# Kernel optimization log

Measured on AMD Instinct MI355X. Metric: run time of the kernel, lower is better.

The kernel has to match this reference:

```python
import jax, jax.numpy as jnp
import numpy as np

B, W, H = 8, 1024, 1024
NUM_LABELS = 100  # mask ids in [0, NUM_LABELS); 0 = background
EPS = 1e-7


def setup_inputs() -> dict:
    key = jax.random.key(0)
    k1, k2 = jax.random.split(key)
    pred = jax.random.normal(k1, (B, 2, W, H), dtype=jnp.float32)
    mask = jax.random.randint(k2, (B, W, H), 0, NUM_LABELS, dtype=jnp.int32)
    ignored_map = jnp.ones((B, W, H), dtype=jnp.float32)
    return {"pred": pred, "mask": mask, "ignored_map": ignored_map}


def _smooth_l1(d):
    # SmoothL1Loss(reduction='none'), beta=1
    a = jnp.abs(d)
    return jnp.where(a < 1.0, 0.5 * d * d, a - 0.5)


def _gt_single(mask2d):
    # Vectorized replacement of the per-instance python loop:
    # segment-mean for centroids, segment-max for the per-instance `norm`.
    seg = mask2d.reshape(-1)  # [W*H]
    x_map = jnp.tile(jnp.arange(H, dtype=jnp.float32), W)    # column index (x)
    y_map = jnp.repeat(jnp.arange(W, dtype=jnp.float32), H)  # row index (y)
    cnt = jax.ops.segment_sum(jnp.ones_like(x_map), seg, num_segments=NUM_LABELS)
    safe_cnt = jnp.maximum(cnt, 1.0)
    xc = (jax.ops.segment_sum(x_map, seg, num_segments=NUM_LABELS) / safe_cnt)[seg]
    yc = (jax.ops.segment_sum(y_map, seg, num_segments=NUM_LABELS) / safe_cnt)[seg]
    fg = (seg != 0).astype(jnp.float32)  # label 0 is background (index_list[1:])
    vx = (x_map - xc) * fg  # (x_map - mean_x) * nuclei, instances are disjoint
    vy = (y_map - yc) * fg
    # torch.max over the whole image of (coord - c)*nuclei == max(seg_max, 0)
    mx = jnp.maximum(jax.ops.segment_max(vx, seg, num_segments=NUM_LABELS), 0.0)
    my = jnp.maximum(jax.ops.segment_max(vy, seg, num_segments=NUM_LABELS), 0.0)
    gx = vx / jnp.where(mx == 0.0, 1.0, mx)[seg]  # norm(): divide by max iff max != 0
    gy = vy / jnp.where(my == 0.0, 1.0, my)[seg]
    return jnp.stack([gx, gy]).reshape(2, W, H)


def reference(pred, mask, ignored_map):
    gt = jax.vmap(_gt_single)(mask)  # [B, 2, W, H]
    fg = (mask != 0).astype(jnp.float32)[:, None]  # [B, 1, W, H]
    bg = 1.0 - fg
    n = float(mask.size)
    # ((mask != 0) + 1e-07).sum() == fg_count + eps * numel
    fg_den = jnp.sum(fg) + EPS * n
    bg_den = jnp.sum(bg) + EPS * n
    d = _smooth_l1(pred - gt)
    ig = ignored_map[:, None]
    offset_loss = jnp.sum(d * ig * (fg / fg_den + bg / bg_den))
    return offset_loss, gt
```

## Files before the change

kernel.cpp:

```cpp
#include <hip/hip_runtime.h>

#define NL 100
#define BB 8
#define WW 1024
#define HH 1024
#define NPIX (WW * WW)
#define EPSF 1e-7f

#define OFF_CNT 0
#define OFF_SX  800
#define OFF_SY  1600
#define OFF_XC  2400
#define OFF_YC  3200
#define OFF_MX  4000
#define OFF_MY  4800
#define OFF_INV 5600
#define WS_WORDS 5602

__global__ __launch_bounds__(256) void k_hist(const int* __restrict__ mask,
                                              int* __restrict__ ws) {
    __shared__ int s_cnt[4][NL];
    __shared__ int s_sx[4][NL];
    __shared__ int s_sy[4][NL];
    const int b  = blockIdx.y;
    const int wv = threadIdx.x >> 6;
    for (int i = threadIdx.x; i < 4 * NL; i += 256) {
        ((int*)s_cnt)[i] = 0; ((int*)s_sx)[i] = 0; ((int*)s_sy)[i] = 0;
    }
    __syncthreads();
    const int4* m4 = (const int4*)(mask + (size_t)b * NPIX);
    const int base4 = blockIdx.x * 1024;
#pragma unroll
    for (int it = 0; it < 4; ++it) {
        const int i4 = base4 + it * 256 + threadIdx.x;
        const int4 mv = m4[i4];
        const int p  = i4 << 2;
        const int x0 = p & (HH - 1);
        const int y  = p >> 10;
        atomicAdd(&s_cnt[wv][mv.x], 1); atomicAdd(&s_sx[wv][mv.x], x0);     atomicAdd(&s_sy[wv][mv.x], y);
        atomicAdd(&s_cnt[wv][mv.y], 1); atomicAdd(&s_sx[wv][mv.y], x0 + 1); atomicAdd(&s_sy[wv][mv.y], y);
        atomicAdd(&s_cnt[wv][mv.z], 1); atomicAdd(&s_sx[wv][mv.z], x0 + 2); atomicAdd(&s_sy[wv][mv.z], y);
        atomicAdd(&s_cnt[wv][mv.w], 1); atomicAdd(&s_sx[wv][mv.w], x0 + 3); atomicAdd(&s_sy[wv][mv.w], y);
    }
    __syncthreads();
    for (int i = threadIdx.x; i < NL; i += 256) {
        const int c = s_cnt[0][i] + s_cnt[1][i] + s_cnt[2][i] + s_cnt[3][i];
        if (c) {
            atomicAdd(&ws[OFF_CNT + b * NL + i], c);
            atomicAdd(&ws[OFF_SX  + b * NL + i], s_sx[0][i] + s_sx[1][i] + s_sx[2][i] + s_sx[3][i]);
            atomicAdd(&ws[OFF_SY  + b * NL + i], s_sy[0][i] + s_sy[1][i] + s_sy[2][i] + s_sy[3][i]);
        }
    }
}

__global__ void k_final(int* __restrict__ wsi) {
    float* wsf = (float*)wsi;
    const int t = threadIdx.x;
    if (t < BB * NL) {
        const int c = wsi[OFF_CNT + t];
        const float sc = (float)(c > 0 ? c : 1);
        wsf[OFF_XC + t] = (float)wsi[OFF_SX + t] / sc;
        wsf[OFF_YC + t] = (float)wsi[OFF_SY + t] / sc;
    }
    if (t == 0) {
        long long bg = 0;
        for (int b = 0; b < BB; ++b) bg += wsi[OFF_CNT + b * NL];
        const float n = (float)BB * (float)NPIX;
        const float fg_den = (float)((long long)BB * NPIX - bg) + EPSF * n;
        const float bg_den = (float)bg + EPSF * n;
        wsf[OFF_INV + 0] = 1.0f / fg_den;
        wsf[OFF_INV + 1] = 1.0f / bg_den;
    }
}

__global__ __launch_bounds__(256) void k_max(const int* __restrict__ mask,
                                             int* __restrict__ ws) {
    const float* wsf = (const float*)ws;
    __shared__ float s_xc[NL], s_yc[NL];
    __shared__ unsigned s_mx[4][NL], s_my[4][NL];
    const int b  = blockIdx.y;
    const int wv = threadIdx.x >> 6;
    for (int i = threadIdx.x; i < NL; i += 256) {
        s_xc[i] = wsf[OFF_XC + b * NL + i];
        s_yc[i] = wsf[OFF_YC + b * NL + i];
    }
    for (int i = threadIdx.x; i < 4 * NL; i += 256) {
        ((unsigned*)s_mx)[i] = 0u; ((unsigned*)s_my)[i] = 0u;
    }
    __syncthreads();
    const int4* m4 = (const int4*)(mask + (size_t)b * NPIX);
    const int base4 = blockIdx.x * 1024;
#pragma unroll
    for (int it = 0; it < 4; ++it) {
        const int i4 = base4 + it * 256 + threadIdx.x;
        const int4 mv = m4[i4];
        const int p  = i4 << 2;
        const float x0 = (float)(p & (HH - 1));
        const float y  = (float)(p >> 10);
        const int mm[4] = {mv.x, mv.y, mv.z, mv.w};
#pragma unroll
        for (int j = 0; j < 4; ++j) {
            const int m = mm[j];
            if (m != 0) {
                const float vx = x0 + (float)j - s_xc[m];
                const float vy = y - s_yc[m];
                if (vx > 0.0f) atomicMax(&s_mx[wv][m], __float_as_uint(vx));
                if (vy > 0.0f) atomicMax(&s_my[wv][m], __float_as_uint(vy));
            }
        }
    }
    __syncthreads();
    for (int i = threadIdx.x; i < NL; i += 256) {
        const unsigned ax = max(max(s_mx[0][i], s_mx[1][i]), max(s_mx[2][i], s_mx[3][i]));
        const unsigned ay = max(max(s_my[0][i], s_my[1][i]), max(s_my[2][i], s_my[3][i]));
        if (ax) atomicMax((unsigned*)&ws[OFF_MX + b * NL + i], ax);
        if (ay) atomicMax((unsigned*)&ws[OFF_MY + b * NL + i], ay);
    }
}

__global__ __launch_bounds__(256) void k_loss(const int* __restrict__ mask,
                                              const float* __restrict__ pred,
                                              const float* __restrict__ ig,
                                              const int* __restrict__ ws,
                                              float* __restrict__ out) {
    const float* wsf = (const float*)ws;
    __shared__ float s_xc[NL], s_yc[NL], s_imx[NL], s_imy[NL];
    const int b = blockIdx.y;
    for (int i = threadIdx.x; i < NL; i += 256) {
        s_xc[i] = wsf[OFF_XC + b * NL + i];
        s_yc[i] = wsf[OFF_YC + b * NL + i];
        const float mx = wsf[OFF_MX + b * NL + i];
        const float my = wsf[OFF_MY + b * NL + i];
        s_imx[i] = (mx == 0.0f) ? 1.0f : 1.0f / mx;
        s_imy[i] = (my == 0.0f) ? 1.0f : 1.0f / my;
    }
    __syncthreads();
    const float inv_fg = wsf[OFF_INV + 0];
    const float inv_bg = wsf[OFF_INV + 1];
    const int4*   m4  = (const int4*)(mask + (size_t)b * NPIX);
    const float4* ig4 = (const float4*)(ig + (size_t)b * NPIX);
    const float4* px4 = (const float4*)(pred + (size_t)(b * 2) * NPIX);
    const float4* py4 = (const float4*)(pred + (size_t)(b * 2 + 1) * NPIX);
    float* gx_out = out + 1 + (size_t)(b * 2) * NPIX;
    float* gy_out = out + 1 + (size_t)(b * 2 + 1) * NPIX;

    float acc = 0.0f;
    const int base4 = blockIdx.x * 1024;
#pragma unroll
    for (int it = 0; it < 4; ++it) {
        const int i4 = base4 + it * 256 + threadIdx.x;
        const int4   mv  = m4[i4];
        const float4 iv  = ig4[i4];
        const float4 pxv = px4[i4];
        const float4 pyv = py4[i4];
        const int p  = i4 << 2;
        const float x0 = (float)(p & (HH - 1));
        const float y  = (float)(p >> 10);
        const int*   mm  = (const int*)&mv;
        const float* igs = (const float*)&iv;
        const float* pxs = (const float*)&pxv;
        const float* pys = (const float*)&pyv;
#pragma unroll
        for (int j = 0; j < 4; ++j) {
            const int m = mm[j];
            float gx = 0.0f, gy = 0.0f, w;
            if (m != 0) {
                gx = (x0 + (float)j - s_xc[m]) * s_imx[m];
                gy = (y - s_yc[m]) * s_imy[m];
                w = inv_fg;
            } else {
                w = inv_bg;
            }
            w *= igs[j];
            const float dx = pxs[j] - gx;
            const float dy = pys[j] - gy;
            const float ax = fabsf(dx), ay = fabsf(dy);
            const float lx = (ax < 1.0f) ? 0.5f * dx * dx : ax - 0.5f;
            const float ly = (ay < 1.0f) ? 0.5f * dy * dy : ay - 0.5f;
            acc += (lx + ly) * w;
            gx_out[p + j] = gx;
            gy_out[p + j] = gy;
        }
    }
#pragma unroll
    for (int off = 32; off > 0; off >>= 1) acc += __shfl_down(acc, off, 64);
    __shared__ float s_part[4];
    const int lane = threadIdx.x & 63, wv = threadIdx.x >> 6;
    if (lane == 0) s_part[wv] = acc;
    __syncthreads();
    if (threadIdx.x == 0) atomicAdd(out, s_part[0] + s_part[1] + s_part[2] + s_part[3]);
}

extern "C" void kernel_launch(void* const* d_in, const int* in_sizes, int n_in,
                              void* d_out, int out_size, void* d_ws, size_t ws_size,
                              hipStream_t stream) {
    const float* pred = (const float*)d_in[0];
    const int*   mask = (const int*)d_in[1];
    const float* ig   = (const float*)d_in[2];
    float* out = (float*)d_out;
    int*   ws  = (int*)d_ws;

    hipMemsetAsync(d_ws, 0, WS_WORDS * sizeof(int), stream);
    hipMemsetAsync(d_out, 0, sizeof(float), stream);

    dim3 grid(256, BB);
    k_hist<<<grid, 256, 0, stream>>>(mask, ws);
    k_final<<<1, 800, 0, stream>>>(ws);
    k_max<<<grid, 256, 0, stream>>>(mask, ws);
    k_loss<<<grid, 256, 0, stream>>>(mask, pred, ig, ws, out);
}
```

Measured before the change: 216.2 us.

## Fold max pass into stats via max(coord)-centroid identity, pack histogram atomics

```diff
diff --git a/kernel.cpp b/kernel.cpp
--- a/kernel.cpp
+++ b/kernel.cpp
@@ -4,52 +4,70 @@
 #define BB 8
 #define WW 1024
 #define HH 1024
-#define NPIX (WW * WW)
+#define NPIX (WW * HH)
 #define EPSF 1e-7f
 
 #define OFF_CNT 0
 #define OFF_SX  800
 #define OFF_SY  1600
-#define OFF_XC  2400
-#define OFF_YC  3200
-#define OFF_MX  4000
-#define OFF_MY  4800
-#define OFF_INV 5600
-#define WS_WORDS 5602
+#define OFF_MX  2400
+#define OFF_MY  3200
+#define OFF_TAB 4000
+#define OFF_INV 7200
+#define WS_WORDS 7202
 
-__global__ __launch_bounds__(256) void k_hist(const int* __restrict__ mask,
-                                              int* __restrict__ ws) {
-    __shared__ int s_cnt[4][NL];
-    __shared__ int s_sx[4][NL];
-    __shared__ int s_sy[4][NL];
+__global__ __launch_bounds__(256) void k_stats(const int* __restrict__ mask,
+                                               int* __restrict__ ws) {
+    __shared__ unsigned long long s_h[4][NL];
+    __shared__ int s_mx[4][NL];
+    __shared__ int s_my[4][NL];
     const int b  = blockIdx.y;
     const int wv = threadIdx.x >> 6;
     for (int i = threadIdx.x; i < 4 * NL; i += 256) {
-        ((int*)s_cnt)[i] = 0; ((int*)s_sx)[i] = 0; ((int*)s_sy)[i] = 0;
+        ((unsigned long long*)s_h)[i] = 0ull;
+        ((int*)s_mx)[i] = 0;
+        ((int*)s_my)[i] = 0;
     }
     __syncthreads();
     const int4* m4 = (const int4*)(mask + (size_t)b * NPIX);
-    const int base4 = blockIdx.x * 1024;
+    const int base4 = blockIdx.x * 2048;
 #pragma unroll
-    for (int it = 0; it < 4; ++it) {
+    for (int it = 0; it < 8; ++it) {
         const int i4 = base4 + it * 256 + threadIdx.x;
         const int4 mv = m4[i4];
         const int p  = i4 << 2;
         const int x0 = p & (HH - 1);
         const int y  = p >> 10;
-        atomicAdd(&s_cnt[wv][mv.x], 1); atomicAdd(&s_sx[wv][mv.x], x0);     atomicAdd(&s_sy[wv][mv.x], y);
-        atomicAdd(&s_cnt[wv][mv.y], 1); atomicAdd(&s_sx[wv][mv.y], x0 + 1); atomicAdd(&s_sy[wv][mv.y], y);
-        atomicAdd(&s_cnt[wv][mv.z], 1); atomicAdd(&s_sx[wv][mv.z], x0 + 2); atomicAdd(&s_sy[wv][mv.z], y);
-        atomicAdd(&s_cnt[wv][mv.w], 1); atomicAdd(&s_sx[wv][mv.w], x0 + 3); atomicAdd(&s_sy[wv][mv.w], y);
+        const int mm[4] = {mv.x, mv.y, mv.z, mv.w};
+#pragma unroll
+        for (int j = 0; j < 4; ++j) {
+            const int m = mm[j];
+            const int x = x0 + j;
+            atomicAdd(&s_h[wv][m],
+                      (1ull << 46) | ((unsigned long long)x << 23) | (unsigned long long)y);
+            if (x > s_mx[wv][m]) atomicMax(&s_mx[wv][m], x);
+            if (y > s_my[wv][m]) atomicMax(&s_my[wv][m], y);
+        }
     }
     __syncthreads();
     for (int i = threadIdx.x; i < NL; i += 256) {
-        const int c = s_cnt[0][i] + s_cnt[1][i] + s_cnt[2][i] + s_cnt[3][i];
+        int c = 0, sx = 0, sy = 0, mx = 0, my = 0;
+#pragma unroll
+        for (int w = 0; w < 4; ++w) {
+            const unsigned long long v = s_h[w][i];
+            c  += (int)(v >> 46);
+            sx += (int)((v >> 23) & 0x7FFFFFull);
+            sy += (int)(v & 0x7FFFFFull);
+            mx = max(mx, s_mx[w][i]);
+            my = max(my, s_my[w][i]);
+        }
         if (c) {
             atomicAdd(&ws[OFF_CNT + b * NL + i], c);
-            atomicAdd(&ws[OFF_SX  + b * NL + i], s_sx[0][i] + s_sx[1][i] + s_sx[2][i] + s_sx[3][i]);
-            atomicAdd(&ws[OFF_SY  + b * NL + i], s_sy[0][i] + s_sy[1][i] + s_sy[2][i] + s_sy[3][i]);
+            atomicAdd(&ws[OFF_SX  + b * NL + i], sx);
+            atomicAdd(&ws[OFF_SY  + b * NL + i], sy);
         }
+        if (mx) atomicMax(&ws[OFF_MX + b * NL + i], mx);
+        if (my) atomicMax(&ws[OFF_MY + b * NL + i], my);
     }
 }
 
@@ -59,8 +77,16 @@
     if (t < BB * NL) {
         const int c = wsi[OFF_CNT + t];
         const float sc = (float)(c > 0 ? c : 1);
-        wsf[OFF_XC + t] = (float)wsi[OFF_SX + t] / sc;
-        wsf[OFF_YC + t] = (float)wsi[OFF_SY + t] / sc;
+        const float xc = (float)wsi[OFF_SX + t] / sc;
+        const float yc = (float)wsi[OFF_SY + t] / sc;
+        float fmx = (float)wsi[OFF_MX + t] - xc; if (fmx < 0.0f) fmx = 0.0f;
+        float fmy = (float)wsi[OFF_MY + t] - yc; if (fmy < 0.0f) fmy = 0.0f;
+        float4 e;
+        e.x = xc;
+        e.y = yc;
+        e.z = (fmx == 0.0f) ? 1.0f : 1.0f / fmx;
+        e.w = (fmy == 0.0f) ? 1.0f : 1.0f / fmy;
+        ((float4*)(wsf + OFF_TAB))[t] = e;
     }
     if (t == 0) {
         long long bg = 0;
@@ -73,115 +99,62 @@
     }
 }
 
-__global__ __launch_bounds__(256) void k_max(const int* __restrict__ mask,
-                                             int* __restrict__ ws) {
-    const float* wsf = (const float*)ws;
-    __shared__ float s_xc[NL], s_yc[NL];
-    __shared__ unsigned s_mx[4][NL], s_my[4][NL];
-    const int b  = blockIdx.y;
-    const int wv = threadIdx.x >> 6;
-    for (int i = threadIdx.x; i < NL; i += 256) {
-        s_xc[i] = wsf[OFF_XC + b * NL + i];
-        s_yc[i] = wsf[OFF_YC + b * NL + i];
-    }
-    for (int i = threadIdx.x; i < 4 * NL; i += 256) {
-        ((unsigned*)s_mx)[i] = 0u; ((unsigned*)s_my)[i] = 0u;
-    }
-    __syncthreads();
-    const int4* m4 = (const int4*)(mask + (size_t)b * NPIX);
-    const int base4 = blockIdx.x * 1024;
-#pragma unroll
-    for (int it = 0; it < 4; ++it) {
-        const int i4 = base4 + it * 256 + threadIdx.x;
-        const int4 mv = m4[i4];
-        const int p  = i4 << 2;
-        const float x0 = (float)(p & (HH - 1));
-        const float y  = (float)(p >> 10);
-        const int mm[4] = {mv.x, mv.y, mv.z, mv.w};
-#pragma unroll
-        for (int j = 0; j < 4; ++j) {
-            const int m = mm[j];
-            if (m != 0) {
-                const float vx = x0 + (float)j - s_xc[m];
-                const float vy = y - s_yc[m];
-                if (vx > 0.0f) atomicMax(&s_mx[wv][m], __float_as_uint(vx));
-                if (vy > 0.0f) atomicMax(&s_my[wv][m], __float_as_uint(vy));
-            }
-        }
-    }
-    __syncthreads();
-    for (int i = threadIdx.x; i < NL; i += 256) {
-        const unsigned ax = max(max(s_mx[0][i], s_mx[1][i]), max(s_mx[2][i], s_mx[3][i]));
-        const unsigned ay = max(max(s_my[0][i], s_my[1][i]), max(s_my[2][i], s_my[3][i]));
-        if (ax) atomicMax((unsigned*)&ws[OFF_MX + b * NL + i], ax);
-        if (ay) atomicMax((unsigned*)&ws[OFF_MY + b * NL + i], ay);
-    }
-}
-
 __global__ __launch_bounds__(256) void k_loss(const int* __restrict__ mask,
                                               const float* __restrict__ pred,
                                               const float* __restrict__ ig,
                                               const int* __restrict__ ws,
                                               float* __restrict__ out) {
     const float* wsf = (const float*)ws;
-    __shared__ float s_xc[NL], s_yc[NL], s_imx[NL], s_imy[NL];
+    __shared__ float4 s_tab[NL];
     const int b = blockIdx.y;
-    for (int i = threadIdx.x; i < NL; i += 256) {
-        s_xc[i] = wsf[OFF_XC + b * NL + i];
-        s_yc[i] = wsf[OFF_YC + b * NL + i];
-        const float mx = wsf[OFF_MX + b * NL + i];
-        const float my = wsf[OFF_MY + b * NL + i];
-        s_imx[i] = (mx == 0.0f) ? 1.0f : 1.0f / mx;
-        s_imy[i] = (my == 0.0f) ? 1.0f : 1.0f / my;
-    }
+    if (threadIdx.x < NL) s_tab[threadIdx.x] = ((const float4*)(wsf + OFF_TAB))[b * NL + threadIdx.x];
     __syncthreads();
     const float inv_fg = wsf[OFF_INV + 0];
     const float inv_bg = wsf[OFF_INV + 1];
-    const int4*   m4  = (const int4*)(mask + (size_t)b * NPIX);
-    const float4* ig4 = (const float4*)(ig + (size_t)b * NPIX);
-    const float4* px4 = (const float4*)(pred + (size_t)(b * 2) * NPIX);
-    const float4* py4 = (const float4*)(pred + (size_t)(b * 2 + 1) * NPIX);
-    float* gx_out = out + 1 + (size_t)(b * 2) * NPIX;
-    float* gy_out = out + 1 + (size_t)(b * 2 + 1) * NPIX;
+
+    const int i4 = blockIdx.x * 256 + threadIdx.x;
+    const int4   mv  = ((const int4*)  (mask + (size_t)b * NPIX))[i4];
+    const float4 iv  = ((const float4*)(ig   + (size_t)b * NPIX))[i4];
+    const float4 pxv = ((const float4*)(pred + (size_t)(2 * b)     * NPIX))[i4];
+    const float4 pyv = ((const float4*)(pred + (size_t)(2 * b + 1) * NPIX))[i4];
+    const int p  = i4 << 2;
+    const float x0 = (float)(p & (HH - 1));
+    const float y  = (float)(p >> 10);
+
+    const int*   mm  = (const int*)&mv;
+    const float* igs = (const float*)&iv;
+    const float* pxs = (const float*)&pxv;
+    const float* pys = (const float*)&pyv;
+    float4 gxv, gyv;
+    float* gxa = (float*)&gxv;
+    float* gya = (float*)&gyv;
 
     float acc = 0.0f;
-    const int base4 = blockIdx.x * 1024;
 #pragma unroll
-    for (int it = 0; it < 4; ++it) {
-        const int i4 = base4 + it * 256 + threadIdx.x;
-        const int4   mv  = m4[i4];
-        const float4 iv  = ig4[i4];
-        const float4 pxv = px4[i4];
-        const float4 pyv = py4[i4];
-        const int p  = i4 << 2;
-        const float x0 = (float)(p & (HH - 1));
-        const float y  = (float)(p >> 10);
-        const int*   mm  = (const int*)&mv;
-        const float* igs = (const float*)&iv;
-        const float* pxs = (const float*)&pxv;
-        const float* pys = (const float*)&pyv;
-#pragma unroll
-        for (int j = 0; j < 4; ++j) {
-            const int m = mm[j];
-            float gx = 0.0f, gy = 0.0f, w;
-            if (m != 0) {
-                gx = (x0 + (float)j - s_xc[m]) * s_imx[m];
-                gy = (y - s_yc[m]) * s_imy[m];
-                w = inv_fg;
-            } else {
-                w = inv_bg;
-            }
-            w *= igs[j];
-            const float dx = pxs[j] - gx;
-            const float dy = pys[j] - gy;
-            const float ax = fabsf(dx), ay = fabsf(dy);
-            const float lx = (ax < 1.0f) ? 0.5f * dx * dx : ax - 0.5f;
-            const float ly = (ay < 1.0f) ? 0.5f * dy * dy : ay - 0.5f;
-            acc += (lx + ly) * w;
-            gx_out[p + j] = gx;
-            gy_out[p + j] = gy;
+    for (int j = 0; j < 4; ++j) {
+        const int m = mm[j];
+        float gx = 0.0f, gy = 0.0f, w;
+        if (m != 0) {
+            const float4 t = s_tab[m];
+            gx = (x0 + (float)j - t.x) * t.z;
+            gy = (y - t.y) * t.w;
+            w = inv_fg;
+        } else {
+            w = inv_bg;
         }
+        w *= igs[j];
+        const float dx = pxs[j] - gx;
+        const float dy = pys[j] - gy;
+        const float ax = fabsf(dx), ay = fabsf(dy);
+        const float lx = (ax < 1.0f) ? 0.5f * dx * dx : ax - 0.5f;
+        const float ly = (ay < 1.0f) ? 0.5f * dy * dy : ay - 0.5f;
+        acc += (lx + ly) * w;
+        gxa[j] = gx;
+        gya[j] = gy;
     }
+    ((float4*)(out + 1 + (size_t)(2 * b)     * NPIX))[i4] = gxv;
+    ((float4*)(out + 1 + (size_t)(2 * b + 1) * NPIX))[i4] = gyv;
+
 #pragma unroll
     for (int off = 32; off > 0; off >>= 1) acc += __shfl_down(acc, off, 64);
     __shared__ float s_part[4];
@@ -203,9 +176,7 @@
     hipMemsetAsync(d_ws, 0, WS_WORDS * sizeof(int), stream);
     hipMemsetAsync(d_out, 0, sizeof(float), stream);
 
-    dim3 grid(256, BB);
-    k_hist<<<grid, 256, 0, stream>>>(mask, ws);
+    k_stats<<<dim3(128, BB), 256, 0, stream>>>(mask, ws);
     k_final<<<1, 800, 0, stream>>>(ws);
-    k_max<<<grid, 256, 0, stream>>>(mask, ws);
-    k_loss<<<grid, 256, 0, stream>>>(mask, pred, ig, ws, out);
+    k_loss<<<dim3(1024, BB), 256, 0, stream>>>(mask, pred, ig, ws, out);
 }
```

Measured after the change: 256.2 us. 1.19x slower.
